# Optimization experiments

Measured on AMD Instinct MI355X. Metric: run time of the kernel, lower is better.

## Reference

```python
import jax, jax.numpy as jnp
import numpy as np

N_NODES = 200000
MAX_DEG = 128
S1, S2 = 25, 10  # neighbor sample sizes per hop (GraphSAGE defaults)


def setup_inputs() -> dict:
    key = jax.random.key(0)
    ks = jax.random.split(key, 9)
    F, H, C, B = 256, 128, 41, 1024
    return {
        "node_ids": jax.random.randint(ks[0], (B,), 0, N_NODES, dtype=jnp.int32),
        "features": jax.random.normal(ks[1], (N_NODES, F), dtype=jnp.float32),
        "adj_info": jax.random.randint(ks[2], (N_NODES, MAX_DEG), 0, N_NODES, dtype=jnp.int32),
        "W_self1": jax.random.normal(ks[3], (F, H), dtype=jnp.float32) * 0.05,
        "W_neigh1": jax.random.normal(ks[4], (F, H), dtype=jnp.float32) * 0.05,
        "W_self2": jax.random.normal(ks[5], (2 * H, H), dtype=jnp.float32) * 0.05,
        "W_neigh2": jax.random.normal(ks[6], (2 * H, H), dtype=jnp.float32) * 0.05,
        "W_pred": jax.random.normal(ks[7], (2 * H, C), dtype=jnp.float32) * 0.05,
        "b_pred": jnp.zeros((C,), dtype=jnp.float32),
    }


def _sample(adj_info, node_ids):
    """Uniform neighbor sampling: hop1 [B,S1], hop2 [B,S1,S2]."""
    k1, k2 = jax.random.split(jax.random.key(42))
    B = node_ids.shape[0]
    cols1 = jax.random.randint(k1, (B, S1), 0, MAX_DEG)
    hop1 = jnp.take_along_axis(adj_info[node_ids], cols1, axis=1)  # [B,S1]
    cols2 = jax.random.randint(k2, (B * S1, S2), 0, MAX_DEG)
    hop2 = jnp.take_along_axis(adj_info[hop1.reshape(-1)], cols2, axis=1)
    return hop1, hop2.reshape(B, S1, S2)


def _mean_agg(self_f, neigh_f, Ws, Wn, act):
    # GraphSAGE MeanAggregator with concat: [self@Ws ; mean(neigh)@Wn]
    neigh = neigh_f.mean(axis=-2)
    return act(jnp.concatenate([self_f @ Ws, neigh @ Wn], axis=-1))


def reference(node_ids, features, adj_info, W_self1, W_neigh1, W_self2, W_neigh2, W_pred, b_pred):
    hop1, hop2 = _sample(adj_info, node_ids)
    f0 = features[node_ids]      # [B,F]
    f1 = features[hop1]          # [B,S1,F]
    f2 = features[hop2]          # [B,S1,S2,F]

    h0 = _mean_agg(f0, f1, W_self1, W_neigh1, jax.nn.relu)   # [B,2H]
    h1 = _mean_agg(f1, f2, W_self1, W_neigh1, jax.nn.relu)   # [B,S1,2H]
    h = _mean_agg(h0, h1, W_self2, W_neigh2, lambda x: x)    # [B,2H]

    # tf.math.l2_normalize(x, 1): x * rsqrt(max(sum(x^2), 1e-12))
    h = h * jax.lax.rsqrt(jnp.maximum(jnp.sum(h * h, axis=1, keepdims=True), 1e-12))
    logits = h @ W_pred + b_pred
    return jax.nn.softmax(logits, axis=-1)
```

## Files before the change

### kernel.cpp

```cpp
#include <hip/hip_runtime.h>
#include <cstdint>
#include <cstddef>

#define BATCH 1024
#define S1 25
#define S2 10
#define FDIM 256
#define HDIM 128
#define NCLS 41
#define MAXDEG 128

typedef __attribute__((ext_vector_type(8))) short bf16x8;
typedef __attribute__((ext_vector_type(4))) float f32x4;

__host__ __device__ static inline void tf2x32(uint32_t k0, uint32_t k1,
                                              uint32_t c0, uint32_t c1,
                                              uint32_t& o0, uint32_t& o1) {
  const uint32_t ks2 = k0 ^ k1 ^ 0x1BD11BDAu;
  uint32_t x0 = c0 + k0, x1 = c1 + k1;
#define TFR(r) { x0 += x1; x1 = (x1 << (r)) | (x1 >> (32 - (r))); x1 ^= x0; }
  TFR(13) TFR(15) TFR(26) TFR(6)
  x0 += k1;  x1 += ks2 + 1u;
  TFR(17) TFR(29) TFR(16) TFR(24)
  x0 += ks2; x1 += k0 + 2u;
  TFR(13) TFR(15) TFR(26) TFR(6)
  x0 += k0;  x1 += k1 + 3u;
  TFR(17) TFR(29) TFR(16) TFR(24)
  x0 += k1;  x1 += ks2 + 4u;
  TFR(13) TFR(15) TFR(26) TFR(6)
  x0 += ks2; x1 += k0 + 5u;
#undef TFR
  o0 = x0; o1 = x1;
}

__device__ static inline uint32_t rand_bits_at(uint32_t kb0, uint32_t kb1, uint32_t j) {
  uint32_t o0, o1;
  tf2x32(kb0, kb1, 0u, j, o0, o1);
  return o0 ^ o1;
}

__device__ static inline ushort f2bf(float x) {
  uint32_t u = __float_as_uint(x);
  return (ushort)((u + 0x7fffu + ((u >> 16) & 1u)) >> 16);
}

__global__ __launch_bounds__(256)
void prep_kernel(const int* __restrict__ node_ids, const float* __restrict__ feat,
                 const int* __restrict__ adj,
                 const float* __restrict__ Ws1, const float* __restrict__ Wn1,
                 int* __restrict__ hop1g, ushort* __restrict__ n2m,
                 float* __restrict__ n1m, ushort* __restrict__ WbT,
                 float* __restrict__ h1m,
                 uint32_t kb1_0, uint32_t kb1_1, uint32_t kb2_0, uint32_t kb2_1) {
  const int blk = blockIdx.x;
  const int t = threadIdx.x;
  if (blk < 6400) {
    const int wave = t >> 6, lane = t & 63;
    const int g = blk * 4 + wave;
    const int b = g / S1;
    int hop1v = 0;
    if (lane == 0) {
      uint32_t c1 = rand_bits_at(kb1_0, kb1_1, (uint32_t)g) & (MAXDEG - 1);
      hop1v = adj[(size_t)node_ids[b] * MAXDEG + c1];
    }
    hop1v = __shfl(hop1v, 0, 64);
    if (lane == 0) hop1g[g] = hop1v;
    int r2id = 0;
    if (lane < S2) {
      uint32_t c2 = rand_bits_at(kb2_0, kb2_1, (uint32_t)(g * S2 + lane)) & (MAXDEG - 1);
      r2id = adj[(size_t)hop1v * MAXDEG + c2];
    }
    float4 acc = make_float4(0.f, 0.f, 0.f, 0.f);
#pragma unroll
    for (int r = 0; r < S2; ++r) {
      int rid = __shfl(r2id, r, 64);
      float4 v = ((const float4*)(feat + (size_t)rid * FDIM))[lane];
      acc.x += v.x; acc.y += v.y; acc.z += v.z; acc.w += v.w;
    }
    const float inv = 1.f / S2;
    ushort4 o;
    o.x = f2bf(acc.x * inv); o.y = f2bf(acc.y * inv);
    o.z = f2bf(acc.z * inv); o.w = f2bf(acc.w * inv);
    *(ushort4*)(n2m + (size_t)g * FDIM + lane * 4) = o;
  } else if (blk < 6656) {
    const int wave = t >> 6, lane = t & 63;
    const int b = (blk - 6400) * 4 + wave;
    int h1v = 0;
    if (lane < S1) {
      uint32_t c1 = rand_bits_at(kb1_0, kb1_1, (uint32_t)(b * S1 + lane)) & (MAXDEG - 1);
      h1v = adj[(size_t)node_ids[b] * MAXDEG + c1];
    }
    float4 acc = make_float4(0.f, 0.f, 0.f, 0.f);
#pragma unroll
    for (int r = 0; r < S1; ++r) {
      int rid = __shfl(h1v, r, 64);
      float4 v = ((const float4*)(feat + (size_t)rid * FDIM))[lane];
      acc.x += v.x; acc.y += v.y; acc.z += v.z; acc.w += v.w;
    }
    const float inv = 1.f / S1;
    acc.x *= inv; acc.y *= inv; acc.z *= inv; acc.w *= inv;
    ((float4*)(n1m + (size_t)b * FDIM))[lane] = acc;
  } else if (blk < 6912) {
    const int idx = blk - 6656;
    const int h = idx >> 7, n = idx & 127;
    const float* W = h ? Wn1 : Ws1;
    WbT[(size_t)idx * FDIM + t] = f2bf(W[(size_t)t * HDIM + n]);
  } else {
    const int i = (blk - 6912) * 256 + t;
    ((float4*)h1m)[i] = make_float4(0.f, 0.f, 0.f, 0.f);
  }
}

__global__ __launch_bounds__(256, 2)
void mfma_h1_kernel(const int* __restrict__ hop1g, const float* __restrict__ feat,
                    const ushort* __restrict__ n2m, const ushort* __restrict__ WbT,
                    float* __restrict__ h1m) {
  const int half = blockIdx.y;
  const ushort* Bmat = WbT + (size_t)half * HDIM * FDIM;
  const int m0 = blockIdx.x * 64;
  const int tid = threadIdx.x;
  const int wave = tid >> 6;
  const int lane = tid & 63;
  const int lq = lane >> 4;
  const int lr = lane & 15;

  __shared__ ushort As[64][40];
  __shared__ ushort Bs[128][40];
  __shared__ float  Cs[64][132];
  __shared__ int rowid[64];

  if (half == 0 && tid < 64) rowid[tid] = hop1g[m0 + tid];
  __syncthreads();

  f32x4 acc[4][2];
#pragma unroll
  for (int rt = 0; rt < 4; ++rt)
#pragma unroll
    for (int ct = 0; ct < 2; ++ct) acc[rt][ct] = (f32x4)(0.f);

  for (int k0 = 0; k0 < FDIM; k0 += 32) {
    const int row = tid >> 2, kc = (tid & 3) * 8;
    if (half == 0) {
      const float* rp = feat + (size_t)rowid[row] * FDIM + k0 + kc;
      float4 v0 = *(const float4*)rp;
      float4 v1 = *(const float4*)(rp + 4);
      union { ushort u[8]; int4 v; } pk;
      pk.u[0] = f2bf(v0.x); pk.u[1] = f2bf(v0.y); pk.u[2] = f2bf(v0.z); pk.u[3] = f2bf(v0.w);
      pk.u[4] = f2bf(v1.x); pk.u[5] = f2bf(v1.y); pk.u[6] = f2bf(v1.z); pk.u[7] = f2bf(v1.w);
      *(int4*)&As[row][kc] = pk.v;
    } else {
      int4 v = *(const int4*)(n2m + (size_t)(m0 + row) * FDIM + k0 + kc);
      *(int4*)&As[row][kc] = v;
    }
#pragma unroll
    for (int i = 0; i < 2; ++i) {
      int idx = tid + i * 256;
      int n = idx >> 2, kc2 = (idx & 3) * 8;
      int4 v = *(const int4*)(Bmat + (size_t)n * FDIM + k0 + kc2);
      *(int4*)&Bs[n][kc2] = v;
    }
    __syncthreads();

    bf16x8 af[4];
#pragma unroll
    for (int rt = 0; rt < 4; ++rt)
      af[rt] = *(const bf16x8*)&As[rt * 16 + lr][lq * 8];
#pragma unroll
    for (int ct = 0; ct < 2; ++ct) {
      bf16x8 bf = *(const bf16x8*)&Bs[wave * 32 + ct * 16 + lr][lq * 8];
#pragma unroll
      for (int rt = 0; rt < 4; ++rt)
        acc[rt][ct] = __builtin_amdgcn_mfma_f32_16x16x32_bf16(af[rt], bf, acc[rt][ct], 0, 0, 0);
    }
    __syncthreads();
  }

#pragma unroll
  for (int rt = 0; rt < 4; ++rt)
#pragma unroll
    for (int ct = 0; ct < 2; ++ct)
#pragma unroll
      for (int r = 0; r < 4; ++r)
        Cs[rt * 16 + lq * 4 + r][wave * 32 + ct * 16 + lr] = fmaxf(acc[rt][ct][r], 0.f);
  __syncthreads();

  if (tid < 128) {
    const int c = tid;
    const int coff = half * HDIM + c;
    float s = 0.f;
    int curb = m0 / S1;
    for (int m = 0; m < 64; ++m) {
      int b = (m0 + m) / S1;
      if (b != curb) {
        atomicAdd(&h1m[(size_t)curb * (2 * HDIM) + coff], s * (1.f / S1));
        s = 0.f; curb = b;
      }
      s += Cs[m][c];
    }
    atomicAdd(&h1m[(size_t)curb * (2 * HDIM) + coff], s * (1.f / S1));
  }
}

__global__ __launch_bounds__(256)
void tail_kernel(const int* __restrict__ node_ids, const float* __restrict__ feat,
                 const float* __restrict__ n1m, const float* __restrict__ h1m,
                 const float* __restrict__ Ws1, const float* __restrict__ Wn1,
                 const float* __restrict__ Ws2, const float* __restrict__ Wn2,
                 const float* __restrict__ Wp, const float* __restrict__ bp,
                 float* __restrict__ out) {
  const int b0 = blockIdx.x * 4;
  const int t = threadIdx.x;
  const int wave = t >> 6, lane = t & 63;

  __shared__ float A0[4][256];
  __shared__ float A1[4][256];
  __shared__ float H1[4][256];
  __shared__ float H0[4][256];
  __shared__ float HN[4][256];
  __shared__ float red[4][4];
  __shared__ float scl[4];
  __shared__ float lg[4][NCLS];
  __shared__ float sm[4][2];

  {
    const int r = wave;
    const int nid = node_ids[b0 + r];
    ((float4*)A0[r])[lane] = ((const float4*)(feat + (size_t)nid * FDIM))[lane];
    ((float4*)A1[r])[lane] = ((const float4*)(n1m + (size_t)(b0 + r) * FDIM))[lane];
    ((float4*)H1[r])[lane] = ((const float4*)(h1m + (size_t)(b0 + r) * FDIM))[lane];
  }
  __syncthreads();

  const int h = t >> 7, c = t & 127;
  {
    const float* W = h ? Wn1 : Ws1;
    const float* Ap = h ? &A1[0][0] : &A0[0][0];
    float acc[4] = {0.f, 0.f, 0.f, 0.f};
    for (int k4 = 0; k4 < 64; ++k4) {
      float w0 = W[(size_t)(k4 * 4 + 0) * HDIM + c];
      float w1 = W[(size_t)(k4 * 4 + 1) * HDIM + c];
      float w2 = W[(size_t)(k4 * 4 + 2) * HDIM + c];
      float w3 = W[(size_t)(k4 * 4 + 3) * HDIM + c];
#pragma unroll
      for (int r = 0; r < 4; ++r) {
        float4 a = ((const float4*)(Ap + r * 256))[k4];
        acc[r] += a.x * w0 + a.y * w1 + a.z * w2 + a.w * w3;
      }
    }
#pragma unroll
    for (int r = 0; r < 4; ++r) H0[r][t] = fmaxf(acc[r], 0.f);
  }
  __syncthreads();

  float hv[4];
  {
    const float* W = h ? Wn2 : Ws2;
    const float* Ap = h ? &H1[0][0] : &H0[0][0];
    float acc[4] = {0.f, 0.f, 0.f, 0.f};
    for (int k4 = 0; k4 < 64; ++k4) {
      float w0 = W[(size_t)(k4 * 4 + 0) * HDIM + c];
      float w1 = W[(size_t)(k4 * 4 + 1) * HDIM + c];
      float w2 = W[(size_t)(k4 * 4 + 2) * HDIM + c];
      float w3 = W[(size_t)(k4 * 4 + 3) * HDIM + c];
#pragma unroll
      for (int r = 0; r < 4; ++r) {
        float4 a = ((const float4*)(Ap + r * 256))[k4];
        acc[r] += a.x * w0 + a.y * w1 + a.z * w2 + a.w * w3;
      }
    }
#pragma unroll
    for (int r = 0; r < 4; ++r) hv[r] = acc[r];
  }

  {
    float ss[4];
#pragma unroll
    for (int r = 0; r < 4; ++r) ss[r] = hv[r] * hv[r];
#pragma unroll
    for (int off = 32; off; off >>= 1)
#pragma unroll
      for (int r = 0; r < 4; ++r) ss[r] += __shfl_xor(ss[r], off, 64);
    if (lane == 0) {
#pragma unroll
      for (int r = 0; r < 4; ++r) red[wave][r] = ss[r];
    }
  }
  __syncthreads();
  if (t < 4) {
    float tot = red[0][t] + red[1][t] + red[2][t] + red[3][t];
    scl[t] = rsqrtf(fmaxf(tot, 1e-12f));
  }
  __syncthreads();
#pragma unroll
  for (int r = 0; r < 4; ++r) HN[r][t] = hv[r] * scl[r];
  __syncthreads();

  int rr = 0, cc = 0;
  float logit = 0.f;
  if (t < 4 * NCLS) {
    rr = t / NCLS; cc = t - rr * NCLS;
    float acc = bp[cc];
    for (int k = 0; k < 2 * HDIM; ++k) acc += HN[rr][k] * Wp[(size_t)k * NCLS + cc];
    lg[rr][cc] = acc;
    logit = acc;
  }
  __syncthreads();
  if (t < 4) {
    float m = -1e30f;
    for (int i = 0; i < NCLS; ++i) m = fmaxf(m, lg[t][i]);
    float s = 0.f;
    for (int i = 0; i < NCLS; ++i) s += expf(lg[t][i] - m);
    sm[t][0] = m; sm[t][1] = s;
  }
  __syncthreads();
  if (t < 4 * NCLS)
    out[(size_t)(b0 + rr) * NCLS + cc] = expf(logit - sm[rr][0]) / sm[rr][1];
}

extern "C" void kernel_launch(void* const* d_in, const int* in_sizes, int n_in,
                              void* d_out, int out_size, void* d_ws, size_t ws_size,
                              hipStream_t stream) {
  const int*   node_ids = (const int*)d_in[0];
  const float* features = (const float*)d_in[1];
  const int*   adj      = (const int*)d_in[2];
  const float* Ws1      = (const float*)d_in[3];
  const float* Wn1      = (const float*)d_in[4];
  const float* Ws2      = (const float*)d_in[5];
  const float* Wn2      = (const float*)d_in[6];
  const float* Wp       = (const float*)d_in[7];
  const float* bp       = (const float*)d_in[8];
  float* out = (float*)d_out;

  char* ws = (char*)d_ws;
  int*    hop1 = (int*)(ws + 0);
  ushort* n2m  = (ushort*)(ws + 102400);
  ushort* WbT  = (ushort*)(ws + 13209600);
  float*  n1m  = (float*)(ws + 13340672);
  float*  h1m  = (float*)(ws + 14389248);

  uint32_t k1_0, k1_1, k2_0, k2_1, kb1_0, kb1_1, kb2_0, kb2_1;
  tf2x32(0u, 42u, 0u, 0u, k1_0, k1_1);
  tf2x32(0u, 42u, 0u, 1u, k2_0, k2_1);
  tf2x32(k1_0, k1_1, 0u, 1u, kb1_0, kb1_1);
  tf2x32(k2_0, k2_1, 0u, 1u, kb2_0, kb2_1);

  prep_kernel<<<7168, 256, 0, stream>>>(node_ids, features, adj, Ws1, Wn1,
                                        hop1, n2m, n1m, WbT, h1m,
                                        kb1_0, kb1_1, kb2_0, kb2_1);

  dim3 gBig(BATCH * S1 / 64, 2);
  mfma_h1_kernel<<<gBig, 256, 0, stream>>>(hop1, features, n2m, WbT, h1m);

  tail_kernel<<<BATCH / 4, 256, 0, stream>>>(node_ids, features, n1m, h1m,
                                             Ws1, Wn1, Ws2, Wn2, Wp, bp, out);
}
```

Before: 384.0 us.

## Materialize bf16 hop1 features in prep and restructure tail kernel

The hop-1 aggregation blocks in the prep kernel now write each gathered neighbor feature row as bf16 into a dense workspace matrix. The MFMA kernel can then load A tiles contiguously instead of doing indirect fp32 gathers plus conversion, and it drops the rowid staging and its barrier; its occupancy hint is raised to 3 blocks. The tail kernel handles 2 batch rows per block instead of 4, which doubles the block count, and it stages W_pred in shared memory with a 4-way split-K for the logits. The cost is an extra 13 MB bf16 write and re-read, and the tail kernel now reads the weights more times overall.

```diff
diff --git a/kernel.cpp b/kernel.cpp
--- a/kernel.cpp
+++ b/kernel.cpp
@@ -48,8 +48,8 @@
 void prep_kernel(const int* __restrict__ node_ids, const float* __restrict__ feat,
                  const int* __restrict__ adj,
                  const float* __restrict__ Ws1, const float* __restrict__ Wn1,
-                 int* __restrict__ hop1g, ushort* __restrict__ n2m,
-                 float* __restrict__ n1m, ushort* __restrict__ WbT,
+                 ushort* __restrict__ n2m, float* __restrict__ n1m,
+                 ushort* __restrict__ f1b, ushort* __restrict__ WbT,
                  float* __restrict__ h1m,
                  uint32_t kb1_0, uint32_t kb1_1, uint32_t kb2_0, uint32_t kb2_1) {
   const int blk = blockIdx.x;
@@ -64,7 +64,6 @@
       hop1v = adj[(size_t)node_ids[b] * MAXDEG + c1];
     }
     hop1v = __shfl(hop1v, 0, 64);
-    if (lane == 0) hop1g[g] = hop1v;
     int r2id = 0;
     if (lane < S2) {
       uint32_t c2 = rand_bits_at(kb2_0, kb2_1, (uint32_t)(g * S2 + lane)) & (MAXDEG - 1);
@@ -96,6 +95,9 @@
       int rid = __shfl(h1v, r, 64);
       float4 v = ((const float4*)(feat + (size_t)rid * FDIM))[lane];
       acc.x += v.x; acc.y += v.y; acc.z += v.z; acc.w += v.w;
+      ushort4 o;
+      o.x = f2bf(v.x); o.y = f2bf(v.y); o.z = f2bf(v.z); o.w = f2bf(v.w);
+      *(ushort4*)(f1b + (size_t)(b * S1 + r) * FDIM + lane * 4) = o;
     }
     const float inv = 1.f / S1;
     acc.x *= inv; acc.y *= inv; acc.z *= inv; acc.w *= inv;
@@ -111,11 +113,11 @@
   }
 }
 
-__global__ __launch_bounds__(256, 2)
-void mfma_h1_kernel(const int* __restrict__ hop1g, const float* __restrict__ feat,
-                    const ushort* __restrict__ n2m, const ushort* __restrict__ WbT,
-                    float* __restrict__ h1m) {
+__global__ __launch_bounds__(256, 3)
+void mfma_h1_kernel(const ushort* __restrict__ f1b, const ushort* __restrict__ n2m,
+                    const ushort* __restrict__ WbT, float* __restrict__ h1m) {
   const int half = blockIdx.y;
+  const ushort* Amat = half ? n2m : f1b;
   const ushort* Bmat = WbT + (size_t)half * HDIM * FDIM;
   const int m0 = blockIdx.x * 64;
   const int tid = threadIdx.x;
@@ -127,10 +129,6 @@
   __shared__ ushort As[64][40];
   __shared__ ushort Bs[128][40];
   __shared__ float  Cs[64][132];
-  __shared__ int rowid[64];
-
-  if (half == 0 && tid < 64) rowid[tid] = hop1g[m0 + tid];
-  __syncthreads();
 
   f32x4 acc[4][2];
 #pragma unroll
@@ -140,16 +138,8 @@
 
   for (int k0 = 0; k0 < FDIM; k0 += 32) {
     const int row = tid >> 2, kc = (tid & 3) * 8;
-    if (half == 0) {
-      const float* rp = feat + (size_t)rowid[row] * FDIM + k0 + kc;
-      float4 v0 = *(const float4*)rp;
-      float4 v1 = *(const float4*)(rp + 4);
-      union { ushort u[8]; int4 v; } pk;
-      pk.u[0] = f2bf(v0.x); pk.u[1] = f2bf(v0.y); pk.u[2] = f2bf(v0.z); pk.u[3] = f2bf(v0.w);
-      pk.u[4] = f2bf(v1.x); pk.u[5] = f2bf(v1.y); pk.u[6] = f2bf(v1.z); pk.u[7] = f2bf(v1.w);
-      *(int4*)&As[row][kc] = pk.v;
-    } else {
-      int4 v = *(const int4*)(n2m + (size_t)(m0 + row) * FDIM + k0 + kc);
+    {
+      int4 v = *(const int4*)(Amat + (size_t)(m0 + row) * FDIM + k0 + kc);
       *(int4*)&As[row][kc] = v;
     }
 #pragma unroll
@@ -208,104 +198,111 @@
                  const float* __restrict__ Ws2, const float* __restrict__ Wn2,
                  const float* __restrict__ Wp, const float* __restrict__ bp,
                  float* __restrict__ out) {
-  const int b0 = blockIdx.x * 4;
+  const int b0 = blockIdx.x * 2;
   const int t = threadIdx.x;
   const int wave = t >> 6, lane = t & 63;
 
-  __shared__ float A0[4][256];
-  __shared__ float A1[4][256];
-  __shared__ float H1[4][256];
-  __shared__ float H0[4][256];
-  __shared__ float HN[4][256];
-  __shared__ float red[4][4];
-  __shared__ float scl[4];
-  __shared__ float lg[4][NCLS];
-  __shared__ float sm[4][2];
-
-  {
+  __shared__ float A0[2][256];
+  __shared__ float A1[2][256];
+  __shared__ float H1[2][256];
+  __shared__ float H0[2][256];
+  __shared__ float HN[2][256];
+  __shared__ float WpL[2 * HDIM * NCLS];
+  __shared__ float bpL[NCLS];
+  __shared__ float red[4][2];
+  __shared__ float scl[2];
+  __shared__ float lg[2][48];
+  __shared__ float sm[2][2];
+
+  if (wave < 2) {
     const int r = wave;
     const int nid = node_ids[b0 + r];
     ((float4*)A0[r])[lane] = ((const float4*)(feat + (size_t)nid * FDIM))[lane];
     ((float4*)A1[r])[lane] = ((const float4*)(n1m + (size_t)(b0 + r) * FDIM))[lane];
+  } else {
+    const int r = wave - 2;
     ((float4*)H1[r])[lane] = ((const float4*)(h1m + (size_t)(b0 + r) * FDIM))[lane];
   }
+  for (int i = t; i < (2 * HDIM * NCLS) / 4; i += 256)
+    ((float4*)WpL)[i] = ((const float4*)Wp)[i];
+  if (t < NCLS) bpL[t] = bp[t];
   __syncthreads();
 
   const int h = t >> 7, c = t & 127;
   {
     const float* W = h ? Wn1 : Ws1;
     const float* Ap = h ? &A1[0][0] : &A0[0][0];
-    float acc[4] = {0.f, 0.f, 0.f, 0.f};
+    float acc0 = 0.f, acc1 = 0.f;
+#pragma unroll 4
     for (int k4 = 0; k4 < 64; ++k4) {
       float w0 = W[(size_t)(k4 * 4 + 0) * HDIM + c];
       float w1 = W[(size_t)(k4 * 4 + 1) * HDIM + c];
       float w2 = W[(size_t)(k4 * 4 + 2) * HDIM + c];
       float w3 = W[(size_t)(k4 * 4 + 3) * HDIM + c];
-#pragma unroll
-      for (int r = 0; r < 4; ++r) {
-        float4 a = ((const float4*)(Ap + r * 256))[k4];
-        acc[r] += a.x * w0 + a.y * w1 + a.z * w2 + a.w * w3;
-      }
-    }
-#pragma unroll
-    for (int r = 0; r < 4; ++r) H0[r][t] = fmaxf(acc[r], 0.f);
-  }
-  __syncthreads();
-
-  float hv[4];
+      float4 a0 = ((const float4*)(Ap))[k4];
+      float4 a1 = ((const float4*)(Ap + 256))[k4];
+      acc0 += a0.x * w0 + a0.y * w1 + a0.z * w2 + a0.w * w3;
+      acc1 += a1.x * w0 + a1.y * w1 + a1.z * w2 + a1.w * w3;
+    }
+    H0[0][t] = fmaxf(acc0, 0.f);
+    H0[1][t] = fmaxf(acc1, 0.f);
+  }
+  __syncthreads();
+
+  float hv0, hv1;
   {
     const float* W = h ? Wn2 : Ws2;
     const float* Ap = h ? &H1[0][0] : &H0[0][0];
-    float acc[4] = {0.f, 0.f, 0.f, 0.f};
+    float acc0 = 0.f, acc1 = 0.f;
+#pragma unroll 4
     for (int k4 = 0; k4 < 64; ++k4) {
       float w0 = W[(size_t)(k4 * 4 + 0) * HDIM + c];
       float w1 = W[(size_t)(k4 * 4 + 1) * HDIM + c];
       float w2 = W[(size_t)(k4 * 4 + 2) * HDIM + c];
       float w3 = W[(size_t)(k4 * 4 + 3) * HDIM + c];
-#pragma unroll
-      for (int r = 0; r < 4; ++r) {
-        float4 a = ((const float4*)(Ap + r * 256))[k4];
-        acc[r] += a.x * w0 + a.y * w1 + a.z * w2 + a.w * w3;
-      }
-    }
-#pragma unroll
-    for (int r = 0; r < 4; ++r) hv[r] = acc[r];
+      float4 a0 = ((const float4*)(Ap))[k4];
+      float4 a1 = ((const float4*)(Ap + 256))[k4];
+      acc0 += a0.x * w0 + a0.y * w1 + a0.z * w2 + a0.w * w3;
+      acc1 += a1.x * w0 + a1.y * w1 + a1.z * w2 + a1.w * w3;
+    }
+    hv0 = acc0; hv1 = acc1;
   }
 
   {
-    float ss[4];
-#pragma unroll
-    for (int r = 0; r < 4; ++r) ss[r] = hv[r] * hv[r];
-#pragma unroll
-    for (int off = 32; off; off >>= 1)
-#pragma unroll
-      for (int r = 0; r < 4; ++r) ss[r] += __shfl_xor(ss[r], off, 64);
-    if (lane == 0) {
-#pragma unroll
-      for (int r = 0; r < 4; ++r) red[wave][r] = ss[r];
-    }
-  }
-  __syncthreads();
-  if (t < 4) {
+    float s0 = hv0 * hv0, s1 = hv1 * hv1;
+#pragma unroll
+    for (int off = 32; off; off >>= 1) {
+      s0 += __shfl_xor(s0, off, 64);
+      s1 += __shfl_xor(s1, off, 64);
+    }
+    if (lane == 0) { red[wave][0] = s0; red[wave][1] = s1; }
+  }
+  __syncthreads();
+  if (t < 2) {
     float tot = red[0][t] + red[1][t] + red[2][t] + red[3][t];
     scl[t] = rsqrtf(fmaxf(tot, 1e-12f));
   }
   __syncthreads();
-#pragma unroll
-  for (int r = 0; r < 4; ++r) HN[r][t] = hv[r] * scl[r];
-  __syncthreads();
-
-  int rr = 0, cc = 0;
-  float logit = 0.f;
-  if (t < 4 * NCLS) {
-    rr = t / NCLS; cc = t - rr * NCLS;
-    float acc = bp[cc];
-    for (int k = 0; k < 2 * HDIM; ++k) acc += HN[rr][k] * Wp[(size_t)k * NCLS + cc];
-    lg[rr][cc] = acc;
-    logit = acc;
-  }
-  __syncthreads();
-  if (t < 4) {
+  HN[0][t] = hv0 * scl[0];
+  HN[1][t] = hv1 * scl[1];
+  __syncthreads();
+
+  {
+    const int g = t >> 2, q = t & 3;
+    for (int p = g; p < 2 * NCLS; p += 64) {
+      const int rr = (p >= NCLS) ? 1 : 0;
+      const int cc = p - rr * NCLS;
+      float s = 0.f;
+#pragma unroll 8
+      for (int k = 0; k < 64; ++k)
+        s += HN[rr][q * 64 + k] * WpL[(size_t)(q * 64 + k) * NCLS + cc];
+      s += __shfl_xor(s, 1, 64);
+      s += __shfl_xor(s, 2, 64);
+      if (q == 0) lg[rr][cc] = s + bpL[cc];
+    }
+  }
+  __syncthreads();
+  if (t < 2) {
     float m = -1e30f;
     for (int i = 0; i < NCLS; ++i) m = fmaxf(m, lg[t][i]);
     float s = 0.f;
@@ -313,8 +310,11 @@
     sm[t][0] = m; sm[t][1] = s;
   }
   __syncthreads();
-  if (t < 4 * NCLS)
-    out[(size_t)(b0 + rr) * NCLS + cc] = expf(logit - sm[rr][0]) / sm[rr][1];
+  if (t < 2 * NCLS) {
+    const int rr = (t >= NCLS) ? 1 : 0;
+    const int cc = t - rr * NCLS;
+    out[(size_t)(b0 + rr) * NCLS + cc] = expf(lg[rr][cc] - sm[rr][0]) / sm[rr][1];
+  }
 }
 
 extern "C" void kernel_launch(void* const* d_in, const int* in_sizes, int n_in,
@@ -332,11 +332,11 @@
   float* out = (float*)d_out;
 
   char* ws = (char*)d_ws;
-  int*    hop1 = (int*)(ws + 0);
-  ushort* n2m  = (ushort*)(ws + 102400);
-  ushort* WbT  = (ushort*)(ws + 13209600);
-  float*  n1m  = (float*)(ws + 13340672);
-  float*  h1m  = (float*)(ws + 14389248);
+  ushort* n2m  = (ushort*)(ws + 0);
+  ushort* f1b  = (ushort*)(ws + 13107200);
+  ushort* WbT  = (ushort*)(ws + 26214400);
+  float*  n1m  = (float*)(ws + 26345472);
+  float*  h1m  = (float*)(ws + 27394048);
 
   uint32_t k1_0, k1_1, k2_0, k2_1, kb1_0, kb1_1, kb2_0, kb2_1;
   tf2x32(0u, 42u, 0u, 0u, k1_0, k1_1);
@@ -345,12 +345,12 @@
   tf2x32(k2_0, k2_1, 0u, 1u, kb2_0, kb2_1);
 
   prep_kernel<<<7168, 256, 0, stream>>>(node_ids, features, adj, Ws1, Wn1,
-                                        hop1, n2m, n1m, WbT, h1m,
+                                        n2m, n1m, f1b, WbT, h1m,
                                         kb1_0, kb1_1, kb2_0, kb2_1);
 
   dim3 gBig(BATCH * S1 / 64, 2);
-  mfma_h1_kernel<<<gBig, 256, 0, stream>>>(hop1, features, n2m, WbT, h1m);
-
-  tail_kernel<<<BATCH / 4, 256, 0, stream>>>(node_ids, features, n1m, h1m,
+  mfma_h1_kernel<<<gBig, 256, 0, stream>>>(f1b, n2m, WbT, h1m);
+
+  tail_kernel<<<BATCH / 2, 256, 0, stream>>>(node_ids, features, n1m, h1m,
                                              Ws1, Wn1, Ws2, Wn2, Wp, bp, out);
 }
```

New measurement: 381.3 us. About the same (-0.7%).
